# Optimization experiments

Measured on AMD Instinct MI355X. Metric: run time of the kernel, lower is better.

The kernel has to match this reference:

```python
import jax, jax.numpy as jnp
import numpy as np

B, S, D, E = 4, 4096, 1024, 8
TOP_K = 2


def setup_inputs() -> dict:
    key = jax.random.key(0)
    k_x, k_gw, k_gb, k_ew, k_eb = jax.random.split(key, 5)
    x = jax.random.normal(k_x, (B, S, D), dtype=jnp.float32)
    gate_w = jax.random.normal(k_gw, (E, D), dtype=jnp.float32) * 0.02
    gate_b = jax.random.normal(k_gb, (E,), dtype=jnp.float32) * 0.02
    expert_w = jax.random.normal(k_ew, (E, D, D), dtype=jnp.float32) * 0.02
    expert_b = jax.random.normal(k_eb, (E, D), dtype=jnp.float32) * 0.02
    return {"x": x, "gate_w": gate_w, "gate_b": gate_b,
            "expert_w": expert_w, "expert_b": expert_b}


def reference(x, gate_w, gate_b, expert_w, expert_b):
    b, s, d = x.shape
    h = x.reshape(-1, d)                                  # [T, D]
    # router: linear -> softmax (fp32) -> top-k -> renormalize
    router_logits = h @ gate_w.T + gate_b                 # [T, E]
    probs = jax.nn.softmax(router_logits.astype(jnp.float32), axis=-1)
    topw, sel = jax.lax.top_k(probs, TOP_K)               # [T, K]
    topw = topw / jnp.sum(topw, axis=-1, keepdims=True)
    topw = topw.astype(h.dtype)
    out = jnp.zeros_like(h)
    for e in range(E):  # small fixed loop over experts
        # per-token combine weight for expert e (0 if not selected)
        we = jnp.sum(jnp.where(sel == e, topw, 0.0), axis=-1)  # [T]
        out = out + (h @ expert_w[e].T + expert_b[e]) * we[:, None]
    return out.reshape(b, s, d), router_logits
```

## Files before the change

kernel.cpp:

```cpp
#include <hip/hip_runtime.h>
#include <hip/hip_bf16.h>

typedef unsigned short u16;
typedef unsigned int u32;

#define T_TOK 16384
#define DIM   1024
#define NEXP  8

#define XB_OFF      0
#define WB_OFF      33554432
#define CNT_OFF     50331648
#define LIST_OFF    50332160
#define SELW_OFF    50856448
#define CONTRIB_OFF 51380736
#define WS_NEED     118489600ULL

__device__ __forceinline__ u16 f2bf(float f) {
    u32 u = __float_as_uint(f);
    u += 0x7fff + ((u >> 16) & 1);
    return (u16)(u >> 16);
}
__device__ __forceinline__ float bf2f(u16 u) {
    return __uint_as_float(((u32)u) << 16);
}

__global__ __launch_bounds__(128) void k_zero(int* counts) {
    if (threadIdx.x < NEXP * 16) counts[threadIdx.x] = 0;
}

#define RT_PB 32

__global__ __launch_bounds__(256) void k_router(
    const float* __restrict__ x, const float* __restrict__ gw,
    const float* __restrict__ gb, float* __restrict__ logits,
    u16* __restrict__ xb, int* __restrict__ counts,
    int* __restrict__ lists, float4* __restrict__ selw,
    const float* __restrict__ ew, u16* __restrict__ wb)
{
    const int tid  = threadIdx.x;
    const int lane = tid & 63;
    const int w    = tid >> 6;

    __shared__ int   s_sel0[RT_PB], s_sel1[RT_PB];
    __shared__ int   s_lcnt[NEXP], s_gbase[NEXP];

    if (tid < NEXP) s_lcnt[tid] = 0;

    for (int i = 0; i < 8; ++i) {
        const int l = w * 8 + i;
        const int t = blockIdx.x * RT_PB + l;

        const float* xr = x + (size_t)t * DIM;
        float4 xs[4];
#pragma unroll
        for (int j = 0; j < 4; ++j)
            xs[j] = *reinterpret_cast<const float4*>(xr + (j * 64 + lane) * 4);

        float acc[NEXP];
#pragma unroll
        for (int e = 0; e < NEXP; ++e) {
            const float* gr = gw + e * DIM;
            float s = 0.f;
#pragma unroll
            for (int j = 0; j < 4; ++j) {
                float4 g = *reinterpret_cast<const float4*>(gr + (j * 64 + lane) * 4);
                s += xs[j].x * g.x + xs[j].y * g.y + xs[j].z * g.z + xs[j].w * g.w;
            }
            acc[e] = s;
        }
#pragma unroll
        for (int off = 1; off < 64; off <<= 1) {
#pragma unroll
            for (int e = 0; e < NEXP; ++e) acc[e] += __shfl_xor(acc[e], off);
        }
#pragma unroll
        for (int e = 0; e < NEXP; ++e) acc[e] += gb[e];

        int i0 = 0; float v0 = acc[0];
#pragma unroll
        for (int e = 1; e < NEXP; ++e) if (acc[e] > v0) { v0 = acc[e]; i0 = e; }
        int i1 = -1; float v1 = -3.4e38f;
#pragma unroll
        for (int e = 0; e < NEXP; ++e) if (e != i0 && acc[e] > v1) { v1 = acc[e]; i1 = e; }
        float e1  = __expf(v1 - v0);
        float inv = 1.f / (1.f + e1);
        float w0 = inv, w1 = e1 * inv;

        u16* xrow = xb + (size_t)t * DIM;
#pragma unroll
        for (int j = 0; j < 4; ++j) {
            int c = (j * 64 + lane) * 4;
            float4 v = xs[j];
            ushort4 u;
            u.x = f2bf(v.x); u.y = f2bf(v.y); u.z = f2bf(v.z); u.w = f2bf(v.w);
            *reinterpret_cast<ushort4*>(xrow + c) = u;
        }
        if (lane == 0) {
            float4 lo = make_float4(acc[0], acc[1], acc[2], acc[3]);
            float4 hi = make_float4(acc[4], acc[5], acc[6], acc[7]);
            *reinterpret_cast<float4*>(logits + (size_t)t * NEXP)     = lo;
            *reinterpret_cast<float4*>(logits + (size_t)t * NEXP + 4) = hi;
            selw[t] = make_float4(__int_as_float(i0), __int_as_float(i1), w0, w1);
            s_sel0[l] = i0; s_sel1[l] = i1;
        }
    }
    __syncthreads();

    int i0 = 0, i1 = 0, r0 = 0, r1 = 0;
    if (tid < RT_PB) {
        i0 = s_sel0[tid]; i1 = s_sel1[tid];
        r0 = atomicAdd(&s_lcnt[i0], 1);
        r1 = atomicAdd(&s_lcnt[i1], 1);
    }
    __syncthreads();
    if (tid < NEXP)
        s_gbase[tid] = atomicAdd(&counts[tid * 16], s_lcnt[tid]);
    __syncthreads();
    if (tid < RT_PB) {
        int t  = blockIdx.x * RT_PB + tid;
        lists[i0 * T_TOK + s_gbase[i0] + r0] = t * 2;
        lists[i1 * T_TOK + s_gbase[i1] + r1] = t * 2 + 1;
    }

    const int n4 = NEXP * DIM * DIM / 4;
    const int stride = gridDim.x * 256;
    for (int i = blockIdx.x * 256 + tid; i < n4; i += stride) {
        float4 v = reinterpret_cast<const float4*>(ew)[i];
        ushort4 u;
        u.x = f2bf(v.x); u.y = f2bf(v.y); u.z = f2bf(v.z); u.w = f2bf(v.w);
        reinterpret_cast<ushort4*>(wb)[i] = u;
    }
}


typedef __attribute__((ext_vector_type(8))) short bf16x8;
typedef __attribute__((ext_vector_type(4))) float f32x4;

#define GLDS16(g, l) __builtin_amdgcn_global_load_lds( \
    (const __attribute__((address_space(1))) void*)(g), \
    (__attribute__((address_space(3))) void*)(l), 16, 0, 0)

#define BAR() __builtin_amdgcn_s_barrier()
#define PRIO1() __builtin_amdgcn_s_setprio(1)
#define PRIO0() __builtin_amdgcn_s_setprio(0)
#define VMW4() asm volatile("s_waitcnt vmcnt(4)" ::: "memory")
#define VMW0() asm volatile("s_waitcnt vmcnt(0)" ::: "memory")

template<int ATOMIC>
__global__ __launch_bounds__(256, 2) void k_gemm(
    const u16* __restrict__ xb, const u16* __restrict__ wb,
    const int* __restrict__ counts, const int* __restrict__ lists,
    const float4* __restrict__ selw, u16* __restrict__ contrib,
    float* __restrict__ out)
{
    __shared__ u16 lds[32768];

    const int bid = blockIdx.x;
    const int e   = bid >> 10;
    const int mt  = (bid >> 3) & 127;
    const int nt  = bid & 7;
    const int cnt = counts[e * 16];
    if (mt * 128 >= cnt) return;

    const int tid  = threadIdx.x;
    const int lane = tid & 63;
    const int wid  = tid >> 6;
    const int wm   = wid >> 1;
    const int wn   = wid & 1;
    const int listbase = e * T_TOK;

    const int srow = tid >> 2;
    const int cA   = (((tid & 3) - (tid >> 3)) & 3) * 8;
    int tokA[2];
#pragma unroll
    for (int l = 0; l < 2; ++l) {
        int slot = mt * 128 + l * 64 + srow;
        tokA[l] = lists[listbase + (slot < cnt ? slot : cnt - 1)] >> 1;
    }
    const u16* srcA0 = xb + (size_t)tokA[0] * DIM + cA;
    const u16* srcA1 = xb + (size_t)tokA[1] * DIM + cA;
    const u16* srcB0 = wb + ((size_t)e << 20) + (size_t)(nt * 128 + srow) * DIM + cA;
    const u16* srcB1 = srcB0 + (size_t)64 * DIM;

#define STAGE(nb, ks, kk) do { \
    GLDS16(srcA0 + (kk) + (ks) * 32, &lds[(nb) * 16384 + (ks) * 4096 + wid * 512]); \
    GLDS16(srcA1 + (kk) + (ks) * 32, &lds[(nb) * 16384 + (ks) * 4096 + 2048 + wid * 512]); \
    GLDS16(srcB0 + (kk) + (ks) * 32, &lds[(nb) * 16384 + 8192 + (ks) * 4096 + wid * 512]); \
    GLDS16(srcB1 + (kk) + (ks) * 32, &lds[(nb) * 16384 + 8192 + (ks) * 4096 + 2048 + wid * 512]); } while (0)

    const int cs8  = (((lane >> 4) + ((lane >> 1) & 3)) & 3) * 8;
    const int offA = (wm * 64 + (lane & 15)) * 32 + cs8;
    const int offB = 8192 + (wn * 64 + (lane & 15)) * 32 + cs8;

    bf16x8 Af[4], Bf[4];
    f32x4 acc[4][4];
#pragma unroll
    for (int mi = 0; mi < 4; ++mi)
#pragma unroll
        for (int ni = 0; ni < 4; ++ni) acc[mi][ni] = (f32x4)0.f;

#define LDA4(buf, ks) do { \
    Af[0] = *(const bf16x8*)&lds[(buf) * 16384 + (ks) * 4096 + 0 * 512 + offA]; \
    Af[1] = *(const bf16x8*)&lds[(buf) * 16384 + (ks) * 4096 + 1 * 512 + offA]; \
    Af[2] = *(const bf16x8*)&lds[(buf) * 16384 + (ks) * 4096 + 2 * 512 + offA]; \
    Af[3] = *(const bf16x8*)&lds[(buf) * 16384 + (ks) * 4096 + 3 * 512 + offA]; } while (0)
#define LDB4(buf, ks) do { \
    Bf[0] = *(const bf16x8*)&lds[(buf) * 16384 + (ks) * 4096 + 0 * 512 + offB]; \
    Bf[1] = *(const bf16x8*)&lds[(buf) * 16384 + (ks) * 4096 + 1 * 512 + offB]; \
    Bf[2] = *(const bf16x8*)&lds[(buf) * 16384 + (ks) * 4096 + 2 * 512 + offB]; \
    Bf[3] = *(const bf16x8*)&lds[(buf) * 16384 + (ks) * 4096 + 3 * 512 + offB]; } while (0)
#define MFMA_ROW(i) do { \
    acc[i][0] = __builtin_amdgcn_mfma_f32_16x16x32_bf16(Af[i], Bf[0], acc[i][0], 0, 0, 0); \
    acc[i][1] = __builtin_amdgcn_mfma_f32_16x16x32_bf16(Af[i], Bf[1], acc[i][1], 0, 0, 0); \
    acc[i][2] = __builtin_amdgcn_mfma_f32_16x16x32_bf16(Af[i], Bf[2], acc[i][2], 0, 0, 0); \
    acc[i][3] = __builtin_amdgcn_mfma_f32_16x16x32_bf16(Af[i], Bf[3], acc[i][3], 0, 0, 0); } while (0)
#define MFMA16() do { MFMA_ROW(0); MFMA_ROW(1); MFMA_ROW(2); MFMA_ROW(3); } while (0)

    STAGE(0, 0, 0); STAGE(0, 1, 0);
    VMW4(); BAR();

    for (int t = 0; t < 15; ++t) {
        const int buf = t & 1, nb = buf ^ 1;
        const int kn  = (t + 1) * 64;
        STAGE(nb, 0, kn);
        LDA4(buf, 0); LDB4(buf, 0);
        PRIO1(); MFMA16(); PRIO0();
        VMW4(); BAR();
        STAGE(nb, 1, kn);
        LDA4(buf, 1); LDB4(buf, 1);
        PRIO1(); MFMA16(); PRIO0();
        VMW4(); BAR();
    }
    {
        LDA4(1, 0); LDB4(1, 0);
        PRIO1(); MFMA16(); PRIO0();
        VMW0(); BAR();
        LDA4(1, 1); LDB4(1, 1);
        PRIO1(); MFMA16(); PRIO0();
    }

    const int rbase = (lane >> 4) * 4;
    const int cbase = nt * 128 + wn * 64 + (lane & 15);
#pragma unroll
    for (int mi = 0; mi < 4; ++mi) {
#pragma unroll
        for (int r = 0; r < 4; ++r) {
            int slot = mt * 128 + wm * 64 + mi * 16 + rbase + r;
            if (slot < cnt) {
                int lv = lists[listbase + slot];
                if (ATOMIC) {
                    int tok = lv >> 1;
                    float4 sw = selw[tok];
                    float wgt = (lv & 1) ? sw.w : sw.z;
                    float* orow = out + (size_t)tok * DIM + cbase;
#pragma unroll
                    for (int ni = 0; ni < 4; ++ni)
                        atomicAdd(orow + ni * 16, acc[mi][ni][r] * wgt);
                } else {
                    u16* crow = contrib + (size_t)lv * DIM + cbase;
#pragma unroll
                    for (int ni = 0; ni < 4; ++ni)
                        crow[ni * 16] = f2bf(acc[mi][ni][r]);
                }
            }
        }
    }
}

__global__ __launch_bounds__(256) void k_combine(
    const u16* __restrict__ contrib, const float4* __restrict__ selw,
    const float* __restrict__ eb, float* __restrict__ out)
{
    const int lane = threadIdx.x & 63;
    const int t    = blockIdx.x * 4 + (threadIdx.x >> 6);
    float4 sw = selw[t];
    const int e0 = __float_as_int(sw.x);
    const int e1 = __float_as_int(sw.y);
    const float w0 = sw.z, w1 = sw.w;
    const u16* c0 = contrib + (size_t)(t * 2) * DIM;
    const u16* c1 = c0 + DIM;
    const float* b0 = eb + e0 * DIM;
    const float* b1 = eb + e1 * DIM;
    float* orow = out + (size_t)t * DIM;
#pragma unroll
    for (int j = 0; j < 2; ++j) {
        const int c = (j * 64 + lane) * 8;
        uint4 u0 = *reinterpret_cast<const uint4*>(c0 + c);
        uint4 u1 = *reinterpret_cast<const uint4*>(c1 + c);
        const u16* p0 = (const u16*)&u0;
        const u16* p1 = (const u16*)&u1;
#pragma unroll
        for (int h = 0; h < 2; ++h) {
            float4 bb0 = *reinterpret_cast<const float4*>(b0 + c + h * 4);
            float4 bb1 = *reinterpret_cast<const float4*>(b1 + c + h * 4);
            float4 o;
            o.x = w0 * (bf2f(p0[h*4+0]) + bb0.x) + w1 * (bf2f(p1[h*4+0]) + bb1.x);
            o.y = w0 * (bf2f(p0[h*4+1]) + bb0.y) + w1 * (bf2f(p1[h*4+1]) + bb1.y);
            o.z = w0 * (bf2f(p0[h*4+2]) + bb0.z) + w1 * (bf2f(p1[h*4+2]) + bb1.z);
            o.w = w0 * (bf2f(p0[h*4+3]) + bb0.w) + w1 * (bf2f(p1[h*4+3]) + bb1.w);
            *reinterpret_cast<float4*>(orow + c + h * 4) = o;
        }
    }
}

__global__ __launch_bounds__(256) void k_bias(
    const float4* __restrict__ selw, const float* __restrict__ eb,
    float* __restrict__ out)
{
    const int lane = threadIdx.x & 63;
    const int t    = blockIdx.x * 4 + (threadIdx.x >> 6);
    float4 sw = selw[t];
    const float* b0 = eb + __float_as_int(sw.x) * DIM;
    const float* b1 = eb + __float_as_int(sw.y) * DIM;
    float* orow = out + (size_t)t * DIM;
#pragma unroll
    for (int j = 0; j < 4; ++j) {
        int c = (j * 64 + lane) * 4;
        float4 f0 = *reinterpret_cast<const float4*>(b0 + c);
        float4 f1 = *reinterpret_cast<const float4*>(b1 + c);
        float4 o;
        o.x = sw.z * f0.x + sw.w * f1.x;
        o.y = sw.z * f0.y + sw.w * f1.y;
        o.z = sw.z * f0.z + sw.w * f1.z;
        o.w = sw.z * f0.w + sw.w * f1.w;
        *reinterpret_cast<float4*>(orow + c) = o;
    }
}

extern "C" void kernel_launch(void* const* d_in, const int* in_sizes, int n_in,
                              void* d_out, int out_size, void* d_ws, size_t ws_size,
                              hipStream_t stream) {
    const float* x  = (const float*)d_in[0];
    const float* gw = (const float*)d_in[1];
    const float* gb = (const float*)d_in[2];
    const float* ew = (const float*)d_in[3];
    const float* eb = (const float*)d_in[4];

    float* out    = (float*)d_out;
    float* logits = out + (size_t)T_TOK * DIM;

    char*   ws      = (char*)d_ws;
    u16*    xb      = (u16*)(ws + XB_OFF);
    u16*    wb      = (u16*)(ws + WB_OFF);
    int*    counts  = (int*)(ws + CNT_OFF);
    int*    lists   = (int*)(ws + LIST_OFF);
    float4* selw    = (float4*)(ws + SELW_OFF);
    u16*    contrib = (u16*)(ws + CONTRIB_OFF);

    k_zero<<<1, 128, 0, stream>>>(counts);
    k_router<<<T_TOK / RT_PB, 256, 0, stream>>>(x, gw, gb, logits, xb, counts,
                                                lists, selw, ew, wb);

    const int grid = NEXP * 128 * 8;
    if (ws_size >= WS_NEED) {
        k_gemm<0><<<grid, 256, 0, stream>>>(xb, wb, counts, lists, selw, contrib, out);
        k_combine<<<T_TOK / 4, 256, 0, stream>>>(contrib, selw, eb, out);
    } else {
        k_bias<<<T_TOK / 4, 256, 0, stream>>>(selw, eb, out);
        k_gemm<1><<<grid, 256, 0, stream>>>(xb, wb, counts, lists, selw, contrib, out);
    }
}
```

Measured before the change: 177.3 us.

## Halve LDS tile to 32-wide K stages, raise occupancy, remap block order

Shrinks the shared-memory footprint from two 64-wide K buffers to two 32-wide K buffers, rewriting the main loop as a simple double-buffered loop over 32 steps with a full vmcnt(0) wait each step. Launch bounds go from 2 to 4 blocks per CU to hide latency through occupancy instead of deeper prefetch. Block indices are also permuted so consecutive blocks span different experts, which changes L2 reuse of weights and token rows. The risks are more barriers per K, shallower prefetch, and register pressure from the 4-block bound, which could cause spills with 64 accumulator floats per thread.

```diff
diff --git a/kernel.cpp b/kernel.cpp
--- a/kernel.cpp
+++ b/kernel.cpp
@@ -144,19 +144,18 @@
 #define BAR() __builtin_amdgcn_s_barrier()
 #define PRIO1() __builtin_amdgcn_s_setprio(1)
 #define PRIO0() __builtin_amdgcn_s_setprio(0)
-#define VMW4() asm volatile("s_waitcnt vmcnt(4)" ::: "memory")
 #define VMW0() asm volatile("s_waitcnt vmcnt(0)" ::: "memory")
 
 template<int ATOMIC>
-__global__ __launch_bounds__(256, 2) void k_gemm(
+__global__ __launch_bounds__(256, 4) void k_gemm(
     const u16* __restrict__ xb, const u16* __restrict__ wb,
     const int* __restrict__ counts, const int* __restrict__ lists,
     const float4* __restrict__ selw, u16* __restrict__ contrib,
     float* __restrict__ out)
 {
-    __shared__ u16 lds[32768];
-
-    const int bid = blockIdx.x;
+    __shared__ u16 lds[16384];
+
+    const int bid = (blockIdx.x & 7) * 1024 + (blockIdx.x >> 3);
     const int e   = bid >> 10;
     const int mt  = (bid >> 3) & 127;
     const int nt  = bid & 7;
@@ -183,15 +182,15 @@
     const u16* srcB0 = wb + ((size_t)e << 20) + (size_t)(nt * 128 + srow) * DIM + cA;
     const u16* srcB1 = srcB0 + (size_t)64 * DIM;
 
-#define STAGE(nb, ks, kk) do { \
-    GLDS16(srcA0 + (kk) + (ks) * 32, &lds[(nb) * 16384 + (ks) * 4096 + wid * 512]); \
-    GLDS16(srcA1 + (kk) + (ks) * 32, &lds[(nb) * 16384 + (ks) * 4096 + 2048 + wid * 512]); \
-    GLDS16(srcB0 + (kk) + (ks) * 32, &lds[(nb) * 16384 + 8192 + (ks) * 4096 + wid * 512]); \
-    GLDS16(srcB1 + (kk) + (ks) * 32, &lds[(nb) * 16384 + 8192 + (ks) * 4096 + 2048 + wid * 512]); } while (0)
+#define STAGE(b, kk) do { \
+    GLDS16(srcA0 + (kk), &lds[(b) * 8192 + wid * 512]); \
+    GLDS16(srcA1 + (kk), &lds[(b) * 8192 + 2048 + wid * 512]); \
+    GLDS16(srcB0 + (kk), &lds[(b) * 8192 + 4096 + wid * 512]); \
+    GLDS16(srcB1 + (kk), &lds[(b) * 8192 + 4096 + 2048 + wid * 512]); } while (0)
 
     const int cs8  = (((lane >> 4) + ((lane >> 1) & 3)) & 3) * 8;
     const int offA = (wm * 64 + (lane & 15)) * 32 + cs8;
-    const int offB = 8192 + (wn * 64 + (lane & 15)) * 32 + cs8;
+    const int offB = 4096 + (wn * 64 + (lane & 15)) * 32 + cs8;
 
     bf16x8 Af[4], Bf[4];
     f32x4 acc[4][4];
@@ -200,16 +199,16 @@
 #pragma unroll
         for (int ni = 0; ni < 4; ++ni) acc[mi][ni] = (f32x4)0.f;
 
-#define LDA4(buf, ks) do { \
-    Af[0] = *(const bf16x8*)&lds[(buf) * 16384 + (ks) * 4096 + 0 * 512 + offA]; \
-    Af[1] = *(const bf16x8*)&lds[(buf) * 16384 + (ks) * 4096 + 1 * 512 + offA]; \
-    Af[2] = *(const bf16x8*)&lds[(buf) * 16384 + (ks) * 4096 + 2 * 512 + offA]; \
-    Af[3] = *(const bf16x8*)&lds[(buf) * 16384 + (ks) * 4096 + 3 * 512 + offA]; } while (0)
-#define LDB4(buf, ks) do { \
-    Bf[0] = *(const bf16x8*)&lds[(buf) * 16384 + (ks) * 4096 + 0 * 512 + offB]; \
-    Bf[1] = *(const bf16x8*)&lds[(buf) * 16384 + (ks) * 4096 + 1 * 512 + offB]; \
-    Bf[2] = *(const bf16x8*)&lds[(buf) * 16384 + (ks) * 4096 + 2 * 512 + offB]; \
-    Bf[3] = *(const bf16x8*)&lds[(buf) * 16384 + (ks) * 4096 + 3 * 512 + offB]; } while (0)
+#define LDA4(b) do { \
+    Af[0] = *(const bf16x8*)&lds[(b) * 8192 + 0 * 512 + offA]; \
+    Af[1] = *(const bf16x8*)&lds[(b) * 8192 + 1 * 512 + offA]; \
+    Af[2] = *(const bf16x8*)&lds[(b) * 8192 + 2 * 512 + offA]; \
+    Af[3] = *(const bf16x8*)&lds[(b) * 8192 + 3 * 512 + offA]; } while (0)
+#define LDB4(b) do { \
+    Bf[0] = *(const bf16x8*)&lds[(b) * 8192 + 0 * 512 + offB]; \
+    Bf[1] = *(const bf16x8*)&lds[(b) * 8192 + 1 * 512 + offB]; \
+    Bf[2] = *(const bf16x8*)&lds[(b) * 8192 + 2 * 512 + offB]; \
+    Bf[3] = *(const bf16x8*)&lds[(b) * 8192 + 3 * 512 + offB]; } while (0)
 #define MFMA_ROW(i) do { \
     acc[i][0] = __builtin_amdgcn_mfma_f32_16x16x32_bf16(Af[i], Bf[0], acc[i][0], 0, 0, 0); \
     acc[i][1] = __builtin_amdgcn_mfma_f32_16x16x32_bf16(Af[i], Bf[1], acc[i][1], 0, 0, 0); \
@@ -217,26 +216,18 @@
     acc[i][3] = __builtin_amdgcn_mfma_f32_16x16x32_bf16(Af[i], Bf[3], acc[i][3], 0, 0, 0); } while (0)
 #define MFMA16() do { MFMA_ROW(0); MFMA_ROW(1); MFMA_ROW(2); MFMA_ROW(3); } while (0)
 
-    STAGE(0, 0, 0); STAGE(0, 1, 0);
-    VMW4(); BAR();
-
-    for (int t = 0; t < 15; ++t) {
-        const int buf = t & 1, nb = buf ^ 1;
-        const int kn  = (t + 1) * 64;
-        STAGE(nb, 0, kn);
-        LDA4(buf, 0); LDB4(buf, 0);
-        PRIO1(); MFMA16(); PRIO0();
-        VMW4(); BAR();
-        STAGE(nb, 1, kn);
-        LDA4(buf, 1); LDB4(buf, 1);
-        PRIO1(); MFMA16(); PRIO0();
-        VMW4(); BAR();
-    }
-    {
-        LDA4(1, 0); LDB4(1, 0);
+    STAGE(0, 0);
+    VMW0(); BAR();
+
+    for (int s = 0; s < 31; ++s) {
+        const int b = s & 1, nb = b ^ 1;
+        STAGE(nb, (s + 1) * 32);
+        LDA4(b); LDB4(b);
         PRIO1(); MFMA16(); PRIO0();
         VMW0(); BAR();
-        LDA4(1, 1); LDB4(1, 1);
+    }
+    {
+        LDA4(1); LDB4(1);
         PRIO1(); MFMA16(); PRIO0();
     }
 
```

After: 162.4 us. 1.09x faster.
